# Kernel optimization log

Measured on AMD Instinct MI355X. Metric: run time of the kernel, lower is better.

Reference implementation:

```python
import jax, jax.numpy as jnp
import numpy as np
from jax import lax

B, Td, To = 32, 800, 400
A, E, V = 256, 512, 8192  # attention_dim, embedding_dim (=2*A for weight tying), vocab
NEG = -1e9


def setup_inputs() -> dict:
    key = jax.random.key(0)
    ks = jax.random.split(key, 10)
    k = jax.random.normal(ks[0], (B, Td, A), jnp.float32)
    v = jax.random.normal(ks[1], (B, Td, A), jnp.float32)
    encoded_lengths = jnp.maximum(jax.random.randint(ks[2], (B,), 0, Td), 1)
    gt = jax.random.randint(ks[3], (B, To), 0, V)
    # embedding table, padding_idx=0 -> row 0 zeroed; tied with output projection
    emb_W = (jax.random.normal(ks[4], (V, E), jnp.float32) * 0.02).at[0].set(0.0)
    W_ih = jax.random.normal(ks[5], (4 * A, E + A), jnp.float32) * 0.05
    W_hh = jax.random.normal(ks[6], (4 * A, A), jnp.float32) * 0.05
    b_ih = jnp.zeros((4 * A,), jnp.float32)
    b_hh = jnp.zeros((4 * A,), jnp.float32)
    char_b = jnp.zeros((V,), jnp.float32)
    # pre-sampled per-step uniforms for the teacher-forcing coin flips
    u = jax.random.uniform(ks[7], (To,), jnp.float32)
    return dict(k=k, v=v, encoded_lengths=encoded_lengths, gt=gt, p_tf=1,
                emb_W=emb_W, W_ih=W_ih, W_hh=W_hh, b_ih=b_ih, b_hh=b_hh,
                char_b=char_b, u=u)


def reference(k, v, encoded_lengths, gt, p_tf, emb_W, W_ih, W_hh, b_ih, b_hh, char_b, u):
    mask = jnp.arange(Td)[None, :] >= encoded_lengths[:, None]  # (B,Td) True = pad

    def step(carry, xs):
        h, c, ctx, pred = carry
        gt_i, u_i = xs
        input_words = jnp.where(u_i < p_tf, gt_i, pred)          # (B,)
        x = emb_W[input_words]                                   # (B,E)
        gates = (jnp.concatenate([x, ctx], -1) @ W_ih.T + b_ih
                 + h @ W_hh.T + b_hh)                             # (B,4A)
        i_, f_, g_, o_ = jnp.split(gates, 4, axis=-1)             # torch gate order
        c = jax.nn.sigmoid(f_) * c + jax.nn.sigmoid(i_) * jnp.tanh(g_)
        h = jax.nn.sigmoid(o_) * jnp.tanh(c)                      # query (B,A)
        energy = jnp.einsum('bta,ba->bt', k, h)                   # (B,Td)
        energy = jnp.where(mask, NEG, energy)
        attn = jax.nn.softmax(energy, axis=1)
        ctx = jnp.einsum('bt,bta->ba', attn, v)                   # (B,A)
        logits = jnp.concatenate([h, ctx], -1) @ emb_W.T + char_b  # (B,V) tied weights
        pred = jnp.argmax(logits, -1)
        return (h, c, ctx, pred), logits

    init = (jnp.zeros((B, A), k.dtype), jnp.zeros((B, A), k.dtype),
            jnp.zeros((B, A), k.dtype), jnp.zeros((B,), gt.dtype))
    _, logits_seq = lax.scan(step, init, (gt.T, u))               # (To,B,V)
    return jnp.transpose(logits_seq, (1, 2, 0))                   # (B,V,To)
```

## Files before the change

kernel.cpp:

```cpp
#include <hip/hip_runtime.h>
#include <hip/hip_bf16.h>

#define BB 32
#define TD 800
#define TO 400
#define AA 256
#define EE 512
#define VV 8192
#define G4 1024
#define MM (BB*TO)
#define TP 896
#define NEGI -3.4e38f

__device__ __forceinline__ float sigm(float x){ return 1.f/(1.f+expf(-x)); }

__device__ __forceinline__ float decode_ptf(const void* p){
  int w = *(const int*)p;
  if (w >= 0 && w < 1048576) return (float)w;
  return __int_as_float(w);
}

__device__ __forceinline__ void ast(float* p, float v){
  __hip_atomic_store(p, v, __ATOMIC_RELAXED, __HIP_MEMORY_SCOPE_AGENT);
}
__device__ __forceinline__ float ald(const float* p){
  return __hip_atomic_load(p, __ATOMIC_RELAXED, __HIP_MEMORY_SCOPE_AGENT);
}
__device__ __forceinline__ void sig(uint* p){
  asm volatile("s_waitcnt vmcnt(0)" ::: "memory");
  __hip_atomic_fetch_add(p, 1u, __ATOMIC_RELAXED, __HIP_MEMORY_SCOPE_AGENT);
}
__device__ __forceinline__ uint poll(uint* p){
  return __hip_atomic_fetch_add(p, 0u, __ATOMIC_RELAXED, __HIP_MEMORY_SCOPE_AGENT);
}

__global__ void kprep_w(const float* __restrict__ Wih, const float* __restrict__ Whh,
                        float* __restrict__ WF, float* __restrict__ WihxT){
  int id = blockIdx.x*blockDim.x + threadIdx.x;
  const int total = 8*128*512 + EE*G4;
  for (; id < total; id += gridDim.x*blockDim.x){
    if (id < 8*128*512){
      int kk = id & 511; int rq = id >> 9; int q = rq & 127; int r = rq >> 7;
      int j = ((q>>5)<<8) + (r<<5) + (q&31);
      WF[id] = (kk < AA) ? Wih[j*768 + EE + kk] : Whh[j*AA + (kk-AA)];
    } else {
      int i2 = id - 8*128*512;
      int e = i2 >> 10, j = i2 & 1023;
      WihxT[i2] = Wih[j*768 + e];
    }
  }
}

__global__ void kprep_kT(const float* __restrict__ k, float* __restrict__ kT){
  int id = blockIdx.x*blockDim.x + threadIdx.x;
  const int nk = BB*AA*TP;
  for (; id < nk; id += gridDim.x*blockDim.x){
    int t = id % TP;
    int rest = id / TP;
    int a = rest & (AA-1);
    int b = rest >> 8;
    kT[id] = (t < TD) ? k[((size_t)b*TD + t)*AA + a] : 0.f;
  }
}

__global__ __launch_bounds__(256) void kxg(const int* __restrict__ gt,
                     const float* __restrict__ embW,
                     const float* __restrict__ WihxT, const float* __restrict__ bih,
                     const float* __restrict__ bhh, float* __restrict__ XG8){
  __shared__ float Xs[16][64];
  __shared__ int toks[16];
  const int m0 = blockIdx.x * 16;
  const int j0 = blockIdx.y * 256 + (threadIdx.x & 63)*4;
  const int r0 = (threadIdx.x >> 6) * 4;
  float acc[4][4];
  #pragma unroll
  for (int rr=0;rr<4;++rr){ acc[rr][0]=acc[rr][1]=acc[rr][2]=acc[rr][3]=0.f; }
  if (threadIdx.x < 16) toks[threadIdx.x] = gt[m0 + threadIdx.x];
  __syncthreads();
  for (int kc=0; kc<EE; kc+=64){
    {
      int lr = threadIdx.x >> 4;
      int lq = threadIdx.x & 15;
      const float4 xv = *(const float4*)(embW + (size_t)toks[lr]*EE + kc + lq*4);
      Xs[lr][lq*4+0]=xv.x; Xs[lr][lq*4+1]=xv.y; Xs[lr][lq*4+2]=xv.z; Xs[lr][lq*4+3]=xv.w;
    }
    __syncthreads();
    #pragma unroll 4
    for (int kk=0; kk<64; ++kk){
      const float4 wv = *(const float4*)(WihxT + (size_t)(kc+kk)*G4 + j0);
      #pragma unroll
      for (int rr=0;rr<4;++rr){
        float xs = Xs[r0+rr][kk];
        acc[rr][0] += wv.x*xs; acc[rr][1] += wv.y*xs;
        acc[rr][2] += wv.z*xs; acc[rr][3] += wv.w*xs;
      }
    }
    __syncthreads();
  }
  const float4 b1 = *(const float4*)(bih + j0);
  const float4 b2 = *(const float4*)(bhh + j0);
  const int g  = j0 >> 8;
  const int rr8 = (j0 >> 5) & 7;
  const int al = j0 & 31;
  #pragma unroll
  for (int rr=0;rr<4;++rr){
    float4 o4 = make_float4(acc[rr][0]+b1.x+b2.x, acc[rr][1]+b1.y+b2.y,
                            acc[rr][2]+b1.z+b2.z, acc[rr][3]+b1.w+b2.w);
    int m = m0 + r0 + rr;
    *(float4*)(XG8 + ((size_t)m*8 + rr8)*128 + g*32 + al) = o4;
  }
}

__global__ __launch_bounds__(1024) void kseq8(
    const float* __restrict__ kT, const float* __restrict__ v,
    const int* __restrict__ enc, const void* __restrict__ ptfp,
    const float* __restrict__ WF, const float* __restrict__ embW,
    const float* __restrict__ charb, const float* __restrict__ u,
    const float* __restrict__ XG8, const float* __restrict__ WihxT,
    const float* __restrict__ bih, const float* __restrict__ bhh,
    float* __restrict__ HC, float* __restrict__ Hx, float* __restrict__ Ex,
    uint* __restrict__ cnt)
{
  __shared__ float kTl[256*128];
  __shared__ float s_hc[EE];
  __shared__ float part[8*128];
  __shared__ float cpart[4*256];
  __shared__ float e_s[128];
  __shared__ float c_s[32];
  __shared__ float red[16];
  __shared__ float wr_s[8];
  __shared__ float Ssum;
  __shared__ float x_s[512];
  __shared__ float xq_s[128];
  __shared__ float rv[16];
  __shared__ int   ri[16];
  __shared__ int   pred_s;

  const int blk = blockIdx.x;
  const int r = blk & 7;
  const int b = blk >> 3;
  const int tid = threadIdx.x;
  const int len = enc[b];
  const int c4 = (((len + 7) >> 3) + 3) & ~3;
  const int t0 = r*c4;
  const int t1 = min(t0 + c4, len);
  const int tn = max(0, t1 - t0);
  const float ptf = decode_ptf(ptfp);
  uint* mycnt = cnt + b*32;

  for (int i = tid; i < 256*32; i += 1024){
    int a = i >> 5, q4 = i & 31;
    float4 x = *(const float4*)(kT + ((size_t)b*AA + a)*TP + t0 + q4*4);
    *(float4*)(&kTl[a*128 + q4*4]) = x;
  }
  if (tid < 512) s_hc[tid] = 0.f;
  if (tid < 32)  c_s[tid] = 0.f;
  if (tid == 0)  pred_s = 0;
  __syncthreads();

  uint bar_target = 0;

  for (int t=0; t<TO; ++t){
    const int m = b*TO + t;
    const bool tf = (u[t] < ptf);

    float xg0=0.f, xg1=0.f, xg2=0.f, xg3=0.f;
    if (tf){
      if (tid < 32){
        const float* xb = XG8 + ((size_t)m*8 + r)*128;
        xg0 = xb[tid]; xg1 = xb[32+tid]; xg2 = xb[64+tid]; xg3 = xb[96+tid];
      }
    } else {
      for (int i=tid; i<512; i+=1024) x_s[i] = embW[(size_t)pred_s*EE + i];
      __syncthreads();
      if (tid < 128){
        int q = tid;
        int j = ((q>>5)<<8) + (r<<5) + (q&31);
        float a0 = bih[j] + bhh[j];
        for (int e=0;e<EE;++e) a0 += x_s[e]*WihxT[(size_t)e*G4 + j];
        xq_s[q] = a0;
      }
      __syncthreads();
    }

    {
      const int q = tid & 127, kq = tid >> 7;
      const float4* wp = (const float4*)(WF + ((size_t)r*128 + q)*512) + kq*16;
      const float* sp = s_hc + kq*64;
      float ac0=0.f, ac1=0.f, ac2=0.f, ac3=0.f;
      #pragma unroll
      for (int i=0;i<8;++i){
        float4 w0 = wp[2*i], w1 = wp[2*i+1];
        float s0=sp[8*i+0], s1=sp[8*i+1], s2=sp[8*i+2], s3=sp[8*i+3];
        float s4=sp[8*i+4], s5=sp[8*i+5], s6=sp[8*i+6], s7=sp[8*i+7];
        ac0 = fmaf(w0.x,s0,ac0); ac1 = fmaf(w0.y,s1,ac1);
        ac2 = fmaf(w0.z,s2,ac2); ac3 = fmaf(w0.w,s3,ac3);
        ac0 = fmaf(w1.x,s4,ac0); ac1 = fmaf(w1.y,s5,ac1);
        ac2 = fmaf(w1.z,s6,ac2); ac3 = fmaf(w1.w,s7,ac3);
      }
      part[kq*128 + q] = (ac0+ac1)+(ac2+ac3);
    }
    __syncthreads();

    if (tid < 32){
      float gi, gf, gg, go;
      if (tf){ gi=xg0; gf=xg1; gg=xg2; go=xg3; }
      else   { gi=xq_s[tid]; gf=xq_s[32+tid]; gg=xq_s[64+tid]; go=xq_s[96+tid]; }
      #pragma unroll
      for (int kq=0;kq<8;++kq){
        const float* pp = part + kq*128;
        gi += pp[tid]; gf += pp[32+tid]; gg += pp[64+tid]; go += pp[96+tid];
      }
      float cn = sigm(gf)*c_s[tid] + sigm(gi)*tanhf(gg);
      float hn = sigm(go)*tanhf(cn);
      c_s[tid] = cn;
      HC[(size_t)m*EE + r*32 + tid] = hn;
      ast(Hx + b*256 + r*32 + tid, hn);
    }
    bar_target += 8;
    __syncthreads();
    if (tid == 0){
      sig(mycnt);
      while (poll(mycnt) < bar_target) __builtin_amdgcn_s_sleep(1);
    }
    __syncthreads();

    if (tid < 256) s_hc[256 + tid] = ald(Hx + b*256 + tid);
    __syncthreads();

    {
      const int tq = tid & 127, aq = tid >> 7;
      const float* kp = kTl + (aq*32)*128 + tq;
      const float* hp = s_hc + 256 + aq*32;
      float ac0=0.f, ac1=0.f, ac2=0.f, ac3=0.f;
      #pragma unroll
      for (int i=0;i<8;++i){
        float k0 = kp[(4*i+0)*128], h0 = hp[4*i+0];
        float k1 = kp[(4*i+1)*128], h1 = hp[4*i+1];
        float k2 = kp[(4*i+2)*128], h2 = hp[4*i+2];
        float k3 = kp[(4*i+3)*128], h3 = hp[4*i+3];
        ac0 = fmaf(k0,h0,ac0); ac1 = fmaf(k1,h1,ac1);
        ac2 = fmaf(k2,h2,ac2); ac3 = fmaf(k3,h3,ac3);
      }
      part[aq*128 + tq] = (ac0+ac1)+(ac2+ac3);
    }
    __syncthreads();

    if (tid < 128){
      float ev = NEGI;
      if (tid < tn){
        ev = 0.f;
        #pragma unroll
        for (int q=0;q<8;++q) ev += part[q*128 + tid];
      }
      e_s[tid] = ev;
    }
    __syncthreads();
    if (tid < 64){
      float a = fmaxf(e_s[tid], e_s[64+tid]);
      #pragma unroll
      for (int o=1;o<64;o<<=1) a = fmaxf(a, __shfl_xor(a,o));
      if (tid == 0) red[0] = a;
    }
    __syncthreads();
    const float m_i = red[0];
    if (tid < 128) e_s[tid] = expf(e_s[tid] - m_i);
    __syncthreads();
    if (tid < 64){
      float a = e_s[tid] + e_s[64+tid];
      #pragma unroll
      for (int o=1;o<64;o<<=1) a += __shfl_xor(a,o);
      if (tid == 0) red[1] = a;
    }
    __syncthreads();

    {
      const int a = tid & 255, g = tid >> 8;
      float acc = 0.f;
      for (int tt = g; tt < tn; tt += 4){
        acc = fmaf(e_s[tt], v[((size_t)b*TD + t0 + tt)*AA + a], acc);
      }
      cpart[g*256 + a] = acc;
    }
    __syncthreads();
    {
      float* exr = Ex + ((size_t)b*8 + r)*260;
      if (tid < 256){
        float cp = cpart[tid] + cpart[256+tid] + cpart[512+tid] + cpart[768+tid];
        ast(exr + 2 + tid, cp);
      }
      if (tid == 0){ ast(exr + 0, m_i); ast(exr + 1, red[1]); }
    }
    bar_target += 8;
    __syncthreads();
    if (tid == 0){
      sig(mycnt);
      while (poll(mycnt) < bar_target) __builtin_amdgcn_s_sleep(1);
    }
    __syncthreads();

    if (tid < 16){
      int i = tid & 7;
      red[tid] = ald(Ex + ((size_t)b*8 + i)*260 + (tid >> 3));
    }
    __syncthreads();
    if (tid == 0){
      float M = red[0];
      #pragma unroll
      for (int i=1;i<8;++i) M = fmaxf(M, red[i]);
      float S = 0.f;
      #pragma unroll
      for (int i=0;i<8;++i){
        float w = expf(red[i] - M);
        wr_s[i] = w;
        S += w * red[8+i];
      }
      Ssum = S;
    }
    __syncthreads();
    if (tid < 256){
      float* exb = Ex + (size_t)b*8*260 + 2 + tid;
      float c0 = ald(exb + 0*260), c1 = ald(exb + 1*260);
      float c2 = ald(exb + 2*260), c3 = ald(exb + 3*260);
      float c4v= ald(exb + 4*260), c5 = ald(exb + 5*260);
      float c6 = ald(exb + 6*260), c7 = ald(exb + 7*260);
      float cc = wr_s[0]*c0 + wr_s[1]*c1 + wr_s[2]*c2 + wr_s[3]*c3
               + wr_s[4]*c4v + wr_s[5]*c5 + wr_s[6]*c6 + wr_s[7]*c7;
      float cv = cc / Ssum;
      s_hc[tid] = cv;
      if ((tid >> 5) == r) HC[(size_t)m*EE + 256 + tid] = cv;
    }
    __syncthreads();

    const bool need_pred = (t+1 < TO) && !(u[t+1] < ptf);
    if (need_pred){
      const int lane = tid & 63, wvi = tid >> 6;
      float bvv = -3.4e38f; int bii = 0;
      for (int rr=0; rr<8; ++rr){
        int vg = tid*8 + rr;
        float a2 = charb[vg];
        const float* er = embW + (size_t)vg*EE;
        for (int e=0;e<AA;++e) a2 += er[e]*s_hc[256+e];
        for (int e=0;e<AA;++e) a2 += er[AA+e]*s_hc[e];
        if (a2 > bvv){ bvv=a2; bii=vg; }
      }
      #pragma unroll
      for (int o=1;o<64;o<<=1){
        float ov = __shfl_xor(bvv,o); int oi = __shfl_xor(bii,o);
        if (ov > bvv || (ov == bvv && oi < bii)){ bvv=ov; bii=oi; }
      }
      if (lane==0){ rv[wvi]=bvv; ri[wvi]=bii; }
      __syncthreads();
      if (tid==0){
        float fv=rv[0]; int fi=ri[0];
        for (int w2=1;w2<16;++w2){
          if (rv[w2]>fv || (rv[w2]==fv && ri[w2]<fi)){ fv=rv[w2]; fi=ri[w2]; }
        }
        pred_s = fi;
      }
      __syncthreads();
    }
  }
}

__global__ __launch_bounds__(256) void ktrans(const float* __restrict__ HC,
                                              float* __restrict__ HCT){
  __shared__ float tile[64][65];
  const int mb = blockIdx.x;
  const int eb = blockIdx.y;
  const int rr = threadIdx.x >> 4;
  const int cq = threadIdx.x & 15;
  #pragma unroll
  for (int r0=0; r0<64; r0+=16){
    float4 x = *(const float4*)(HC + (size_t)(mb*64+r0+rr)*EE + eb*64 + cq*4);
    tile[r0+rr][cq*4+0]=x.x; tile[r0+rr][cq*4+1]=x.y;
    tile[r0+rr][cq*4+2]=x.z; tile[r0+rr][cq*4+3]=x.w;
  }
  __syncthreads();
  #pragma unroll
  for (int r0=0; r0<64; r0+=16){
    int e = r0 + rr;
    float4 y = make_float4(tile[cq*4+0][e], tile[cq*4+1][e],
                           tile[cq*4+2][e], tile[cq*4+3][e]);
    *(float4*)(HCT + (size_t)(eb*64+e)*MM + mb*64 + cq*4) = y;
  }
}

__global__ __launch_bounds__(256) void klogits(const float* __restrict__ HCT,
      const float* __restrict__ embW, const float* __restrict__ charb,
      float* __restrict__ out)
{
  __shared__ float Ws[64][68];
  const int vb = blockIdx.x;
  const int mb = blockIdx.y;
  const int tid = threadIdx.x;
  const int m = mb*256 + tid;
  float acc[64];
  #pragma unroll
  for (int i=0;i<64;++i) acc[i]=0.f;
  for (int kc=0; kc<EE; kc+=64){
    {
      int v0 = tid >> 2;
      int q  = tid & 3;
      const float4* src = (const float4*)(embW + (size_t)(vb*64+v0)*EE + kc + q*16);
      float4 a4 = src[0], b4 = src[1], c4 = src[2], d4 = src[3];
      int k0 = q*16;
      Ws[k0+ 0][v0]=a4.x; Ws[k0+ 1][v0]=a4.y; Ws[k0+ 2][v0]=a4.z; Ws[k0+ 3][v0]=a4.w;
      Ws[k0+ 4][v0]=b4.x; Ws[k0+ 5][v0]=b4.y; Ws[k0+ 6][v0]=b4.z; Ws[k0+ 7][v0]=b4.w;
      Ws[k0+ 8][v0]=c4.x; Ws[k0+ 9][v0]=c4.y; Ws[k0+10][v0]=c4.z; Ws[k0+11][v0]=c4.w;
      Ws[k0+12][v0]=d4.x; Ws[k0+13][v0]=d4.y; Ws[k0+14][v0]=d4.z; Ws[k0+15][v0]=d4.w;
    }
    __syncthreads();
    for (int kk=0;kk<64;++kk){
      float x = HCT[(size_t)(kc+kk)*MM + m];
      const float4* wr = (const float4*)(&Ws[kk][0]);
      #pragma unroll
      for (int i4=0;i4<16;++i4){
        float4 w4 = wr[i4];
        acc[i4*4+0] += x*w4.x; acc[i4*4+1] += x*w4.y;
        acc[i4*4+2] += x*w4.z; acc[i4*4+3] += x*w4.w;
      }
    }
    __syncthreads();
  }
  const int bb = m / TO;
  const int tt = m - bb*TO;
  #pragma unroll 4
  for (int vv2=0; vv2<64; ++vv2){
    int vg = vb*64 + vv2;
    float rres = acc[vv2] + charb[vg];
    out[((size_t)bb*VV + vg)*TO + tt] = rres;
  }
}

extern "C" void kernel_launch(void* const* d_in, const int* in_sizes, int n_in,
                              void* d_out, int out_size, void* d_ws, size_t ws_size,
                              hipStream_t stream)
{
  const float* k    = (const float*)d_in[0];
  const float* v    = (const float*)d_in[1];
  const int*   enc  = (const int*)d_in[2];
  const int*   gt   = (const int*)d_in[3];
  const void*  ptf  = d_in[4];
  const float* embW = (const float*)d_in[5];
  const float* Wih  = (const float*)d_in[6];
  const float* Whh  = (const float*)d_in[7];
  const float* bih  = (const float*)d_in[8];
  const float* bhh  = (const float*)d_in[9];
  const float* chb  = (const float*)d_in[10];
  const float* u    = (const float*)d_in[11];
  float* out = (float*)d_out;

  float* ws   = (float*)d_ws;
  uint*  cnt  = (uint*)ws;
  float* Hx   = ws + 1024;
  float* Ex   = Hx + (size_t)BB*256;
  float* XG8  = Ex + (size_t)BB*8*260;
  float* HC   = XG8 + (size_t)MM*G4;
  float* WihxT= HC  + (size_t)MM*EE;
  float* WF   = WihxT + (size_t)EE*G4;
  float* kT   = WF + (size_t)8*128*512;
  float* HCT  = XG8;

  hipMemsetAsync(cnt, 0, 1024*sizeof(uint), stream);
  kprep_w  <<<1024, 256, 0, stream>>>(Wih, Whh, WF, WihxT);
  kprep_kT <<<8192, 256, 0, stream>>>(k, kT);
  kxg      <<<dim3(800,4), 256, 0, stream>>>(gt, embW, WihxT, bih, bhh, XG8);
  kseq8    <<<256, 1024, 0, stream>>>(kT, v, enc, ptf, WF, embW, chb, u,
                                      XG8, WihxT, bih, bhh, HC, Hx, Ex, cnt);
  ktrans   <<<dim3(200,8), 256, 0, stream>>>(HC, HCT);
  klogits  <<<dim3(128,50), 256, 0, stream>>>(HCT, embW, chb, out);
}
```

Baseline: 8.043 ms.

## Compute output logits with bf16 MFMA instead of FP32 FMA GEMM

Replaces the transpose-plus-scalar-FP32 logits GEMM with a conversion pass that writes HC and the embedding table as bf16, followed by a matrix-core kernel using 16x16x32 bf16 MFMA. The transpose kernel is dropped because the MFMA kernel reads row-major operands directly. This cuts the vector-ALU cost of the large M x V x E GEMM, at the price of bf16 rounding of both operands, which could change argmax-free logits beyond tolerance. Loads come straight from global memory with no LDS staging, and output stores are strided by TO.

```diff
diff --git a/kernel.cpp b/kernel.cpp
--- a/kernel.cpp
+++ b/kernel.cpp
@@ -12,7 +12,16 @@
 #define TP 896
 #define NEGI -3.4e38f
 
+typedef __attribute__((ext_vector_type(8))) short bf16x8;
+typedef __attribute__((ext_vector_type(4))) float f32x4;
+
 __device__ __forceinline__ float sigm(float x){ return 1.f/(1.f+expf(-x)); }
+
+__device__ __forceinline__ ushort f2bf(float x){
+  uint u = __float_as_uint(x);
+  u += 0x7fffu + ((u >> 16) & 1u);
+  return (ushort)(u >> 16);
+}
 
 __device__ __forceinline__ float decode_ptf(const void* p){
   int w = *(const int*)p;
@@ -363,73 +372,69 @@
   }
 }
 
-__global__ __launch_bounds__(256) void ktrans(const float* __restrict__ HC,
-                                              float* __restrict__ HCT){
-  __shared__ float tile[64][65];
+__global__ void kcvt(const float* __restrict__ HC, const float* __restrict__ embW,
+                     ushort* __restrict__ HCb, ushort* __restrict__ embB){
+  int id = blockIdx.x*blockDim.x + threadIdx.x;
+  const int n1 = MM*EE;
+  const int n2 = VV*EE;
+  for (; id < n1 + n2; id += gridDim.x*blockDim.x){
+    if (id < n1){
+      HCb[id] = f2bf(HC[id]);
+    } else {
+      int i2 = id - n1;
+      embB[i2] = f2bf(embW[i2]);
+    }
+  }
+}
+
+__global__ __launch_bounds__(256) void klogits_mfma(
+    const ushort* __restrict__ HCb, const ushort* __restrict__ embB,
+    const float* __restrict__ charb, float* __restrict__ out)
+{
   const int mb = blockIdx.x;
-  const int eb = blockIdx.y;
-  const int rr = threadIdx.x >> 4;
-  const int cq = threadIdx.x & 15;
+  const int vb = blockIdx.y;
+  const int wid = threadIdx.x >> 6;
+  const int lane = threadIdx.x & 63;
+  const int lrow = lane & 15;
+  const int lk   = (lane >> 4) * 8;
+  const int v0 = vb*64 + wid*16;
+  const int m0 = mb*64;
+
+  f32x4 acc0 = {0.f,0.f,0.f,0.f}, acc1 = {0.f,0.f,0.f,0.f};
+  f32x4 acc2 = {0.f,0.f,0.f,0.f}, acc3 = {0.f,0.f,0.f,0.f};
+
+  const ushort* ea = embB + (size_t)(v0 + lrow)*EE + lk;
+  const ushort* h0 = HCb + (size_t)(m0 +      lrow)*EE + lk;
+  const ushort* h1 = HCb + (size_t)(m0 + 16 + lrow)*EE + lk;
+  const ushort* h2 = HCb + (size_t)(m0 + 32 + lrow)*EE + lk;
+  const ushort* h3 = HCb + (size_t)(m0 + 48 + lrow)*EE + lk;
+
+  #pragma unroll 4
+  for (int kc = 0; kc < EE; kc += 32){
+    bf16x8 a  = *(const bf16x8*)(ea + kc);
+    bf16x8 b0 = *(const bf16x8*)(h0 + kc);
+    bf16x8 b1 = *(const bf16x8*)(h1 + kc);
+    bf16x8 b2 = *(const bf16x8*)(h2 + kc);
+    bf16x8 b3 = *(const bf16x8*)(h3 + kc);
+    acc0 = __builtin_amdgcn_mfma_f32_16x16x32_bf16(a, b0, acc0, 0,0,0);
+    acc1 = __builtin_amdgcn_mfma_f32_16x16x32_bf16(a, b1, acc1, 0,0,0);
+    acc2 = __builtin_amdgcn_mfma_f32_16x16x32_bf16(a, b2, acc2, 0,0,0);
+    acc3 = __builtin_amdgcn_mfma_f32_16x16x32_bf16(a, b3, acc3, 0,0,0);
+  }
+
+  const int vbase = v0 + (lane >> 4)*4;
   #pragma unroll
-  for (int r0=0; r0<64; r0+=16){
-    float4 x = *(const float4*)(HC + (size_t)(mb*64+r0+rr)*EE + eb*64 + cq*4);
-    tile[r0+rr][cq*4+0]=x.x; tile[r0+rr][cq*4+1]=x.y;
-    tile[r0+rr][cq*4+2]=x.z; tile[r0+rr][cq*4+3]=x.w;
-  }
-  __syncthreads();
-  #pragma unroll
-  for (int r0=0; r0<64; r0+=16){
-    int e = r0 + rr;
-    float4 y = make_float4(tile[cq*4+0][e], tile[cq*4+1][e],
-                           tile[cq*4+2][e], tile[cq*4+3][e]);
-    *(float4*)(HCT + (size_t)(eb*64+e)*MM + mb*64 + cq*4) = y;
-  }
-}
-
-__global__ __launch_bounds__(256) void klogits(const float* __restrict__ HCT,
-      const float* __restrict__ embW, const float* __restrict__ charb,
-      float* __restrict__ out)
-{
-  __shared__ float Ws[64][68];
-  const int vb = blockIdx.x;
-  const int mb = blockIdx.y;
-  const int tid = threadIdx.x;
-  const int m = mb*256 + tid;
-  float acc[64];
-  #pragma unroll
-  for (int i=0;i<64;++i) acc[i]=0.f;
-  for (int kc=0; kc<EE; kc+=64){
-    {
-      int v0 = tid >> 2;
-      int q  = tid & 3;
-      const float4* src = (const float4*)(embW + (size_t)(vb*64+v0)*EE + kc + q*16);
-      float4 a4 = src[0], b4 = src[1], c4 = src[2], d4 = src[3];
-      int k0 = q*16;
-      Ws[k0+ 0][v0]=a4.x; Ws[k0+ 1][v0]=a4.y; Ws[k0+ 2][v0]=a4.z; Ws[k0+ 3][v0]=a4.w;
-      Ws[k0+ 4][v0]=b4.x; Ws[k0+ 5][v0]=b4.y; Ws[k0+ 6][v0]=b4.z; Ws[k0+ 7][v0]=b4.w;
-      Ws[k0+ 8][v0]=c4.x; Ws[k0+ 9][v0]=c4.y; Ws[k0+10][v0]=c4.z; Ws[k0+11][v0]=c4.w;
-      Ws[k0+12][v0]=d4.x; Ws[k0+13][v0]=d4.y; Ws[k0+14][v0]=d4.z; Ws[k0+15][v0]=d4.w;
-    }
-    __syncthreads();
-    for (int kk=0;kk<64;++kk){
-      float x = HCT[(size_t)(kc+kk)*MM + m];
-      const float4* wr = (const float4*)(&Ws[kk][0]);
-      #pragma unroll
-      for (int i4=0;i4<16;++i4){
-        float4 w4 = wr[i4];
-        acc[i4*4+0] += x*w4.x; acc[i4*4+1] += x*w4.y;
-        acc[i4*4+2] += x*w4.z; acc[i4*4+3] += x*w4.w;
-      }
-    }
-    __syncthreads();
-  }
-  const int bb = m / TO;
-  const int tt = m - bb*TO;
-  #pragma unroll 4
-  for (int vv2=0; vv2<64; ++vv2){
-    int vg = vb*64 + vv2;
-    float rres = acc[vv2] + charb[vg];
-    out[((size_t)bb*VV + vg)*TO + tt] = rres;
+  for (int j=0; j<4; ++j){
+    const f32x4 av = (j==0)?acc0:(j==1)?acc1:(j==2)?acc2:acc3;
+    const int m = m0 + j*16 + (lane & 15);
+    const int bb = m / TO;
+    const int tt = m - bb*TO;
+    float* op = out + (size_t)bb*VV*TO + tt;
+    #pragma unroll
+    for (int i=0;i<4;++i){
+      int vg = vbase + i;
+      op[(size_t)vg*TO] = av[i] + charb[vg];
+    }
   }
 }
 
@@ -460,7 +465,8 @@
   float* WihxT= HC  + (size_t)MM*EE;
   float* WF   = WihxT + (size_t)EE*G4;
   float* kT   = WF + (size_t)8*128*512;
-  float* HCT  = XG8;
+  ushort* HCb = (ushort*)XG8;
+  ushort* embB= HCb + (size_t)MM*EE;
 
   hipMemsetAsync(cnt, 0, 1024*sizeof(uint), stream);
   kprep_w  <<<1024, 256, 0, stream>>>(Wih, Whh, WF, WihxT);
@@ -468,6 +474,6 @@
   kxg      <<<dim3(800,4), 256, 0, stream>>>(gt, embW, WihxT, bih, bhh, XG8);
   kseq8    <<<256, 1024, 0, stream>>>(kT, v, enc, ptf, WF, embW, chb, u,
                                       XG8, WihxT, bih, bhh, HC, Hx, Ex, cnt);
-  ktrans   <<<dim3(200,8), 256, 0, stream>>>(HC, HCT);
-  klogits  <<<dim3(128,50), 256, 0, stream>>>(HCT, embW, chb, out);
-}
+  kcvt     <<<4096, 256, 0, stream>>>(HC, embW, HCb, embB);
+  klogits_mfma <<<dim3(200,128), 256, 0, stream>>>(HCb, embB, chb, out);
+}
```

Measured after the change: 6.470 ms, median of 3. 19.6% less time.
